# Kernel optimization log

Hardware: AMD Instinct MI355X
Metric: run time of the kernel (lower is better)

## Reference

```python
import jax, jax.numpy as jnp
import numpy as np

N, E, D, H, ED = 50000, 800000, 128, 4, 64
C = D // H  # per-head channels
EPS = 1e-5


def setup_inputs() -> dict:
    key = jax.random.key(0)
    ks = jax.random.split(key, 16)
    s = 0.05
    return {
        "x": jax.random.normal(ks[0], (N, D), jnp.float32),
        "edge_index": jax.random.randint(ks[1], (2, E), 0, N, jnp.int64 if jax.config.jax_enable_x64 else jnp.int32),
        "edge_attr": jax.random.normal(ks[2], (E, ED), jnp.float32),
        "Wq": jax.random.normal(ks[3], (D, H * C), jnp.float32) * s,
        "bq": jnp.zeros((H * C,), jnp.float32),
        "Wk": jax.random.normal(ks[4], (D, H * C), jnp.float32) * s,
        "bk": jnp.zeros((H * C,), jnp.float32),
        "Wv": jax.random.normal(ks[5], (D, H * C), jnp.float32) * s,
        "bv": jnp.zeros((H * C,), jnp.float32),
        "We": jax.random.normal(ks[6], (ED, H * C), jnp.float32) * s,  # lin_edge, bias=False
        "Wskip": jax.random.normal(ks[7], (D, H * C), jnp.float32) * s,
        "bskip": jnp.zeros((H * C,), jnp.float32),
        "Wbeta": jax.random.normal(ks[8], (3 * H * C, 1), jnp.float32) * s,  # lin_beta, bias=False
        "gamma": jnp.ones((D,), jnp.float32),
        "beta_ln": jnp.zeros((D,), jnp.float32),
    }


def _transformer_conv(x, src, dst, edge_attr, Wq, bq, Wk, bk, Wv, bv, We, Wskip, bskip, Wbeta):
    q = (x @ Wq + bq).reshape(N, H, C)
    k = (x @ Wk + bk).reshape(N, H, C)
    v = (x @ Wv + bv).reshape(N, H, C)
    e = (edge_attr @ We).reshape(E, H, C)
    k_j = k[src] + e                     # [E,H,C]
    v_j = v[src] + e                     # [E,H,C]
    alpha = jnp.einsum("ehc,ehc->eh", q[dst], k_j) / jnp.sqrt(jnp.float32(C))
    # per-destination softmax over incoming edges
    m = jax.ops.segment_max(alpha, dst, num_segments=N)          # [N,H]
    m = jnp.where(jnp.isfinite(m), m, 0.0)
    a = jnp.exp(alpha - m[dst])
    denom = jax.ops.segment_sum(a, dst, num_segments=N)          # [N,H]
    alpha = a / jnp.where(denom > 0, denom, 1.0)[dst]
    out = jax.ops.segment_sum(alpha[:, :, None] * v_j, dst, num_segments=N)  # [N,H,C]
    out = out.reshape(N, H * C)
    # beta-gated skip (beta=True, root_weight)
    x_r = x @ Wskip + bskip
    b = jax.nn.sigmoid(jnp.concatenate([out, x_r, out - x_r], axis=-1) @ Wbeta)  # [N,1]
    return b * x_r + (1.0 - b) * out


def reference(x, edge_index, edge_attr, Wq, bq, Wk, bk, Wv, bv, We, Wskip, bskip, Wbeta, gamma, beta_ln):
    src, dst = edge_index[0], edge_index[1]
    res = _transformer_conv(x, src, dst, edge_attr, Wq, bq, Wk, bk, Wv, bv, We, Wskip, bskip, Wbeta)
    out = jax.nn.gelu(res, approximate=False) + x
    mu = jnp.mean(out, axis=-1, keepdims=True)
    var = jnp.var(out, axis=-1, keepdims=True)
    return (out - mu) * jax.lax.rsqrt(var + EPS) * gamma + beta_ln
```

## Files before the change

### kernel.cpp

```cpp
#include <hip/hip_runtime.h>
#include <math.h>

#define NN 50000
#define EE 800000

typedef __bf16 bf16x8 __attribute__((ext_vector_type(8)));
typedef float f32x4 __attribute__((ext_vector_type(4)));
typedef float f32x2 __attribute__((ext_vector_type(2)));
typedef unsigned short ushort_t;
typedef unsigned int uint_t;

__device__ inline ushort_t f2bf(float f) {
  uint_t u = __float_as_uint(f);
  uint_t r = (u + 0x7fffu + ((u >> 16) & 1u)) >> 16;
  return (ushort_t)r;
}
__device__ inline float bflo(uint_t u) { return __uint_as_float(u << 16); }
__device__ inline float bfhi(uint_t u) { return __uint_as_float(u & 0xffff0000u); }

__device__ inline uint_t pk4_fp8(float a0, float a1, float a2, float a3) {
  a0 = fminf(fmaxf(a0, -448.f), 448.f);
  a1 = fminf(fmaxf(a1, -448.f), 448.f);
  a2 = fminf(fmaxf(a2, -448.f), 448.f);
  a3 = fminf(fmaxf(a3, -448.f), 448.f);
  uint_t lo = (uint_t)__builtin_amdgcn_cvt_pk_fp8_f32(a0, a1, 0, false) & 0xFFFFu;
  uint_t hi = (uint_t)__builtin_amdgcn_cvt_pk_fp8_f32(a2, a3, 0, false) & 0xFFFFu;
  return lo | (hi << 16);
}

__device__ inline void wave_sync() {
  asm volatile("s_waitcnt lgkmcnt(0)" ::: "memory");
  __builtin_amdgcn_wave_barrier();
}

__global__ __launch_bounds__(256) void k_prepA(const float* __restrict__ Wbeta,
                                               float* __restrict__ wcomb,
                                               int* __restrict__ counts) {
  int b = blockIdx.x;
  int o = threadIdx.x;
  if (b == 0) {
    if (o < 128) {
      wcomb[o]       = Wbeta[o]       + Wbeta[256 + o];
      wcomb[128 + o] = Wbeta[128 + o] - Wbeta[256 + o];
    }
  } else {
    int i = (b - 1) * 256 + o;
    if (i < NN) counts[i] = 0;
  }
}

__global__ __launch_bounds__(256) void k_prepB(
    const float* __restrict__ Wq, const float* __restrict__ Wk,
    const float* __restrict__ Wv, const float* __restrict__ Ws,
    const float* __restrict__ bq, const float* __restrict__ bk,
    const float* __restrict__ bv, const float* __restrict__ bs,
    ushort_t* __restrict__ Wbt, float* __restrict__ bcat,
    const float* __restrict__ We, ushort_t* __restrict__ WebT,
    const int* __restrict__ ei, int* __restrict__ counts) {
  int b = blockIdx.x;
  if (b >= 288) {
    int i = (b - 288) * 256 + threadIdx.x;
    if (i < EE) atomicAdd(&counts[ei[EE + i]], 1);
    return;
  }
  if (b >= 256) {
    int i = (b - 256) * 256 + threadIdx.x;
    int c = i >> 6, k = i & 63;
    WebT[c * 64 + k] = f2bf(We[k * 128 + c]);
    return;
  }
  int i = b * 256 + threadIdx.x;
  int c = i >> 7, k = i & 127;
  float w;
  if (c < 128)      w = Wq[k * 128 + c];
  else if (c < 256) w = Wk[k * 128 + (c - 128)];
  else if (c < 384) w = Wv[k * 128 + (c - 256)];
  else              w = Ws[k * 128 + (c - 384)];
  Wbt[(size_t)c * 128 + k] = f2bf(w);
  if (i < 512) {
    float bb;
    if (i < 128)      bb = bq[i];
    else if (i < 256) bb = bk[i - 128];
    else if (i < 384) bb = bv[i - 256];
    else              bb = bs[i - 384];
    bcat[i] = bb;
  }
}

__global__ __launch_bounds__(256) void k_mm(const float* __restrict__ x,
                                            const ushort_t* __restrict__ Wbt,
                                            const float* __restrict__ bcat,
                                            float* __restrict__ nqx,
                                            ushort_t* __restrict__ kb,
                                            ushort_t* __restrict__ vb) {
  __shared__ ushort_t As[128 * 128];
  __shared__ ushort_t Bs[128 * 128];
  int t = threadIdx.x;
  int rb = blockIdx.x * 128;
  int cb = blockIdx.y * 128;

  for (int q = t; q < 2048; q += 256) {
    int r = q >> 4, j = q & 15;
    int row = rb + r;
    float4 f0 = make_float4(0.f, 0.f, 0.f, 0.f), f1 = f0;
    if (row < NN) {
      const float4* xp = (const float4*)&x[(size_t)row * 128 + j * 8];
      f0 = xp[0]; f1 = xp[1];
    }
    uint_t u0 = (uint_t)f2bf(f0.x) | ((uint_t)f2bf(f0.y) << 16);
    uint_t u1 = (uint_t)f2bf(f0.z) | ((uint_t)f2bf(f0.w) << 16);
    uint_t u2 = (uint_t)f2bf(f1.x) | ((uint_t)f2bf(f1.y) << 16);
    uint_t u3 = (uint_t)f2bf(f1.z) | ((uint_t)f2bf(f1.w) << 16);
    int e = r * 128 + ((j * 8) ^ ((r & 7) << 3));
    *(uint4*)&As[e] = make_uint4(u0, u1, u2, u3);
  }
  for (int q = t; q < 2048; q += 256) {
    int c = q >> 4, j = q & 15;
    uint4 w = *(const uint4*)&Wbt[(size_t)(cb + c) * 128 + j * 8];
    int e = c * 128 + ((j * 8) ^ ((c & 7) << 3));
    *(uint4*)&Bs[e] = w;
  }
  __syncthreads();

  int lane = t & 63;
  int wv = t >> 6;
  int wr = wv >> 1, wc = wv & 1;
  int l15 = lane & 15, l4 = lane >> 4;

  f32x4 acc[4][4];
#pragma unroll
  for (int i = 0; i < 4; ++i)
#pragma unroll
    for (int j = 0; j < 4; ++j) acc[i][j] = (f32x4){0.f, 0.f, 0.f, 0.f};

#pragma unroll
  for (int ks = 0; ks < 4; ++ks) {
    int kbv = ks * 32 + l4 * 8;
    bf16x8 af[4], bfr[4];
#pragma unroll
    for (int i = 0; i < 4; ++i) {
      int r = wr * 64 + i * 16 + l15;
      af[i] = *(const bf16x8*)&As[r * 128 + (kbv ^ ((r & 7) << 3))];
    }
#pragma unroll
    for (int j = 0; j < 4; ++j) {
      int c = wc * 64 + j * 16 + l15;
      bfr[j] = *(const bf16x8*)&Bs[c * 128 + (kbv ^ ((c & 7) << 3))];
    }
#pragma unroll
    for (int i = 0; i < 4; ++i)
#pragma unroll
      for (int j = 0; j < 4; ++j)
        acc[i][j] = __builtin_amdgcn_mfma_f32_16x16x32_bf16(af[i], bfr[j], acc[i][j], 0, 0, 0);
  }

#pragma unroll
  for (int j = 0; j < 4; ++j) {
    int colg = cb + wc * 64 + j * 16 + l15;
    float bv = bcat[colg];
#pragma unroll
    for (int i = 0; i < 4; ++i) {
#pragma unroll
      for (int reg = 0; reg < 4; ++reg) {
        int grow = rb + wr * 64 + i * 16 + l4 * 4 + reg;
        if (grow < NN) {
          float val = acc[i][j][reg] + bv;
          if (cb == 0)        nqx[(size_t)grow * 256 + colg] = val;
          else if (cb == 128) kb[(size_t)grow * 128 + (colg - 128)] = f2bf(val);
          else if (cb == 256) vb[(size_t)grow * 128 + (colg - 256)] = f2bf(val);
          else                nqx[(size_t)grow * 256 + (colg - 256)] = val;
        }
      }
    }
  }
}

__global__ __launch_bounds__(1024) void k_scan(int* __restrict__ counts, int* __restrict__ offsets) {
  __shared__ int wsum[16];
  __shared__ int s_carry;
  int4* counts4 = (int4*)counts;
  int4* offsets4 = (int4*)offsets;
  int t = threadIdx.x, lane = t & 63, w = t >> 6;
  if (t == 0) s_carry = 0;
  __syncthreads();
  for (int base = 0; base < 12500; base += 1024) {
    int idx = base + t;
    int4 v = (idx < 12500) ? counts4[idx] : make_int4(0, 0, 0, 0);
    int e1 = v.x, e2 = e1 + v.y, e3 = e2 + v.z, tot = e3 + v.w;
    int s = tot;
#pragma unroll
    for (int off = 1; off < 64; off <<= 1) {
      int u = __shfl_up(s, off);
      if (lane >= off) s += u;
    }
    if (lane == 63) wsum[w] = s;
    __syncthreads();
    if (t == 0) {
      int ex = s_carry;
#pragma unroll
      for (int i = 0; i < 16; ++i) { int tv = wsum[i]; wsum[i] = ex; ex += tv; }
      s_carry = ex;
    }
    __syncthreads();
    int be = wsum[w] + s - tot;
    if (idx < 12500) {
      int4 o = make_int4(be, be + e1, be + e2, be + e3);
      offsets4[idx] = o;
      counts4[idx] = o;
    }
    __syncthreads();
  }
  if (t == 0) offsets[NN] = s_carry;
}

__global__ __launch_bounds__(256) void k_fillw(const int* __restrict__ ei,
                                               int* __restrict__ cursors,
                                               const float* __restrict__ ea,
                                               const ushort_t* __restrict__ WebT,
                                               int* __restrict__ srcs,
                                               unsigned char* __restrict__ eaWperm) {
  __shared__ ushort_t As[64 * 64];
  __shared__ ushort_t Bs[128 * 64];
  __shared__ int sP[64];
  int t = threadIdx.x;
  int eb = blockIdx.x * 64;

  if (t < 64) {
    int e = eb + t;
    int d = ei[EE + e];
    int p = atomicAdd(&cursors[d], 1);
    sP[t] = p;
    srcs[p] = ei[e];
  }
  for (int q = t; q < 512; q += 256) {
    int r = q >> 3, j = q & 7;
    const float4* xp = (const float4*)&ea[(size_t)(eb + r) * 64 + j * 8];
    float4 f0 = xp[0], f1 = xp[1];
    uint_t u0 = (uint_t)f2bf(f0.x) | ((uint_t)f2bf(f0.y) << 16);
    uint_t u1 = (uint_t)f2bf(f0.z) | ((uint_t)f2bf(f0.w) << 16);
    uint_t u2 = (uint_t)f2bf(f1.x) | ((uint_t)f2bf(f1.y) << 16);
    uint_t u3 = (uint_t)f2bf(f1.z) | ((uint_t)f2bf(f1.w) << 16);
    *(uint4*)&As[r * 64 + ((j * 8) ^ ((r & 7) << 3))] = make_uint4(u0, u1, u2, u3);
  }
  for (int q = t; q < 1024; q += 256) {
    int c = q >> 3, j = q & 7;
    uint4 w = *(const uint4*)&WebT[(size_t)c * 64 + j * 8];
    *(uint4*)&Bs[c * 64 + ((j * 8) ^ ((c & 7) << 3))] = w;
  }
  __syncthreads();

  int lane = t & 63, wv = t >> 6;
  int l15 = lane & 15, l4 = lane >> 4;
  int edge = wv * 16 + l15;

  bf16x8 bfr[2];
#pragma unroll
  for (int ks = 0; ks < 2; ++ks) {
    int kbv = ks * 32 + l4 * 8;
    bfr[ks] = *(const bf16x8*)&As[edge * 64 + (kbv ^ ((edge & 7) << 3))];
  }

  f32x4 acc[8];
#pragma unroll
  for (int i = 0; i < 8; ++i) acc[i] = (f32x4){0.f, 0.f, 0.f, 0.f};

#pragma unroll
  for (int ks = 0; ks < 2; ++ks) {
    int kbv = ks * 32 + l4 * 8;
#pragma unroll
    for (int i = 0; i < 8; ++i) {
      int c = i * 16 + l15;
      bf16x8 af = *(const bf16x8*)&Bs[c * 64 + (kbv ^ ((c & 7) << 3))];
      acc[i] = __builtin_amdgcn_mfma_f32_16x16x32_bf16(af, bfr[ks], acc[i], 0, 0, 0);
    }
  }

  wave_sync();
  uint_t* dst32 = (uint_t*)As;
#pragma unroll
  for (int i = 0; i < 8; ++i)
    dst32[edge * 32 + i * 4 + l4] = pk4_fp8(acc[i][0], acc[i][1], acc[i][2], acc[i][3]);
  wave_sync();

  int el = wv * 16 + (lane >> 2), seg = lane & 3;
  const uint4* srow = (const uint4*)((const unsigned char*)As + el * 128 + seg * 16);
  uint4 lo = srow[0];
  uint4 hi = srow[4];
  int p = sP[el];
  *(uint4*)&eaWperm[(size_t)p * 128 + seg * 16]      = lo;
  *(uint4*)&eaWperm[(size_t)p * 128 + seg * 16 + 64] = hi;
}

__global__ __launch_bounds__(256) void k_attn(
    const float* __restrict__ nqx,
    const ushort_t* __restrict__ kb, const ushort_t* __restrict__ vb,
    const unsigned char* __restrict__ eaWperm,
    const int* __restrict__ offsets, const int* __restrict__ srcs,
    const float* __restrict__ x, const float* __restrict__ wcomb,
    const float* __restrict__ gamma, const float* __restrict__ beta_ln,
    float* __restrict__ out) {
  __shared__ float sQ[4][128];
  __shared__ unsigned char sEA[4][16][144];
  __shared__ float sA[4][64];
  __shared__ int   sS[4][16];

  int t = threadIdx.x, wv = t >> 6, l = t & 63;
  int n = blockIdx.x * 4 + wv;
  int h = l >> 4, m = l & 15;
  int c0 = 2 * l, c1 = c0 + 1;
  const float scale = 0.17677669529663687f;

  const float* nrow = nqx + (size_t)n * 256;
  float2 q2 = *(const float2*)&nrow[c0];
  *(float2*)&sQ[wv][c0] = make_float2(q2.x * scale, q2.y * scale);
  if (l < 16) sS[wv][l] = 0;

  int js = offsets[n], je = offsets[n + 1];
  float acc0 = 0.f, acc1 = 0.f, lsum = 0.f;

  for (int base = js; base < je; base += 16) {
    int nj = je - base; if (nj > 16) nj = 16;
    wave_sync();

    uint4 e0 = {0,0,0,0}, e1 = {0,0,0,0};
    uint4 k0 = {0,0,0,0}, k1 = {0,0,0,0}, k2 = {0,0,0,0}, k3 = {0,0,0,0};
    if (m < nj) {
      int s = srcs[base + m];
      const uint4* erow = (const uint4*)(eaWperm + (size_t)(base + m) * 128 + 32 * h);
      e0 = erow[0]; e1 = erow[1];
      const uint4* krow = (const uint4*)(kb + (size_t)s * 128 + 32 * h);
      k0 = krow[0]; k1 = krow[1]; k2 = krow[2]; k3 = krow[3];
      if (h == 0) sS[wv][m] = s;
    }
    *(uint4*)&sEA[wv][m][32 * h]      = e0;
    *(uint4*)&sEA[wv][m][32 * h + 16] = e1;
    wave_sync();

    float z = 0.f;
    {
      const float* qp = &sQ[wv][32 * h];
      uint_t eu[8] = {e0.x, e0.y, e0.z, e0.w, e1.x, e1.y, e1.z, e1.w};
      uint_t ku[16] = {k0.x, k0.y, k0.z, k0.w, k1.x, k1.y, k1.z, k1.w,
                       k2.x, k2.y, k2.z, k2.w, k3.x, k3.y, k3.z, k3.w};
#pragma unroll
      for (int u = 0; u < 8; ++u) {
        f32x2 elo = __builtin_amdgcn_cvt_pk_f32_fp8(eu[u] & 0xFFFFu, false);
        f32x2 ehi = __builtin_amdgcn_cvt_pk_f32_fp8(eu[u] >> 16, false);
        float4 q4 = *(const float4*)&qp[4 * u];
        z += q4.x * (bflo(ku[2 * u]) + elo.x)
           + q4.y * (bfhi(ku[2 * u]) + elo.y)
           + q4.z * (bflo(ku[2 * u + 1]) + ehi.x)
           + q4.w * (bfhi(ku[2 * u + 1]) + ehi.y);
      }
    }
    float a = (m < nj) ? __expf(z) : 0.0f;
    lsum += a;
    sA[wv][l] = a;
    wave_sync();

    {
      int4 s0 = *(const int4*)&sS[wv][0];
      int4 s1 = *(const int4*)&sS[wv][4];
      f32x4 a0 = *(const f32x4*)&sA[wv][16 * h];
      f32x4 a1 = *(const f32x4*)&sA[wv][16 * h + 4];
      uint_t vv[8];
      int sidx[8] = {s0.x, s0.y, s0.z, s0.w, s1.x, s1.y, s1.z, s1.w};
#pragma unroll
      for (int e = 0; e < 8; ++e)
        vv[e] = *(const uint_t*)(vb + (size_t)sidx[e] * 128 + c0);
#pragma unroll
      for (int e = 0; e < 8; ++e) {
        float ae = (e < 4) ? a0[e] : a1[e - 4];
        uint_t ew = (uint_t)*(const ushort_t*)&sEA[wv][e][2 * l];
        f32x2 ef = __builtin_amdgcn_cvt_pk_f32_fp8(ew, false);
        acc0 += ae * (bflo(vv[e]) + ef.x);
        acc1 += ae * (bfhi(vv[e]) + ef.y);
      }
    }
    if (nj > 8) {
      int4 s2 = *(const int4*)&sS[wv][8];
      int4 s3 = *(const int4*)&sS[wv][12];
      f32x4 a2 = *(const f32x4*)&sA[wv][16 * h + 8];
      f32x4 a3 = *(const f32x4*)&sA[wv][16 * h + 12];
      uint_t vv[8];
      int sidx[8] = {s2.x, s2.y, s2.z, s2.w, s3.x, s3.y, s3.z, s3.w};
#pragma unroll
      for (int e = 0; e < 8; ++e)
        vv[e] = *(const uint_t*)(vb + (size_t)sidx[e] * 128 + c0);
#pragma unroll
      for (int e = 0; e < 8; ++e) {
        float ae = (e < 4) ? a2[e] : a3[e - 4];
        uint_t ew = (uint_t)*(const ushort_t*)&sEA[wv][8 + e][2 * l];
        f32x2 ef = __builtin_amdgcn_cvt_pk_f32_fp8(ew, false);
        acc0 += ae * (bflo(vv[e]) + ef.x);
        acc1 += ae * (bfhi(vv[e]) + ef.y);
      }
    }
  }

  lsum += __shfl_xor(lsum, 1); lsum += __shfl_xor(lsum, 2);
  lsum += __shfl_xor(lsum, 4); lsum += __shfl_xor(lsum, 8);

  float inv = (lsum > 0.f) ? (1.0f / lsum) : 1.0f;
  float o0 = acc0 * inv;
  float o1 = acc1 * inv;

  float2 xrv = *(const float2*)&nrow[128 + c0];
  float bp = o0 * wcomb[c0] + o1 * wcomb[c1] + xrv.x * wcomb[128 + c0] + xrv.y * wcomb[128 + c1];
#pragma unroll
  for (int off = 32; off > 0; off >>= 1) bp += __shfl_xor(bp, off);
  float bgate = 1.0f / (1.0f + __expf(-bp));
  float r0 = bgate * xrv.x + (1.0f - bgate) * o0;
  float r1 = bgate * xrv.y + (1.0f - bgate) * o1;

  float2 xv = *(const float2*)&x[(size_t)n * 128 + c0];
  float ge0 = 0.5f * r0 * (1.0f + erff(r0 * 0.70710678118654752f)) + xv.x;
  float ge1 = 0.5f * r1 * (1.0f + erff(r1 * 0.70710678118654752f)) + xv.y;

  float s1 = ge0 + ge1;
  float s2 = ge0 * ge0 + ge1 * ge1;
#pragma unroll
  for (int off = 32; off > 0; off >>= 1) {
    s1 += __shfl_xor(s1, off);
    s2 += __shfl_xor(s2, off);
  }
  float mean = s1 * (1.0f / 128.0f);
  float var = s2 * (1.0f / 128.0f) - mean * mean;
  float rstd = rsqrtf(var + 1e-5f);
  float2 ov;
  ov.x = (ge0 - mean) * rstd * gamma[c0] + beta_ln[c0];
  ov.y = (ge1 - mean) * rstd * gamma[c1] + beta_ln[c1];
  *(float2*)&out[(size_t)n * 128 + c0] = ov;
}

extern "C" void kernel_launch(void* const* d_in, const int* in_sizes, int n_in,
                              void* d_out, int out_size, void* d_ws, size_t ws_size,
                              hipStream_t stream) {
  const float* x   = (const float*)d_in[0];
  const int*   ei  = (const int*)d_in[1];
  const float* ea  = (const float*)d_in[2];
  const float* Wq  = (const float*)d_in[3];
  const float* bq  = (const float*)d_in[4];
  const float* Wk  = (const float*)d_in[5];
  const float* bk  = (const float*)d_in[6];
  const float* Wv  = (const float*)d_in[7];
  const float* bv  = (const float*)d_in[8];
  const float* We  = (const float*)d_in[9];
  const float* Wsk = (const float*)d_in[10];
  const float* bsk = (const float*)d_in[11];
  const float* Wb  = (const float*)d_in[12];
  const float* gamma = (const float*)d_in[13];
  const float* beta  = (const float*)d_in[14];
  float* out = (float*)d_out;

  char* cur = (char*)d_ws;
  auto alloc = [&](size_t bytes) {
    void* p = (void*)cur;
    cur += (bytes + 255) & ~(size_t)255;
    return p;
  };
  float*         nqx     = (float*)alloc((size_t)NN * 256 * 4);
  ushort_t*      kbuf    = (ushort_t*)alloc((size_t)NN * 128 * 2);
  ushort_t*      vbuf    = (ushort_t*)alloc((size_t)NN * 128 * 2);
  unsigned char* eaWperm = (unsigned char*)alloc((size_t)EE * 128);
  int*           srcs    = (int*)alloc((size_t)EE * 4);
  float*         wcomb   = (float*)alloc(256 * 4);
  float*         bcat    = (float*)alloc(512 * 4);
  ushort_t*      Wbt     = (ushort_t*)alloc((size_t)512 * 128 * 2);
  ushort_t*      WebT    = (ushort_t*)alloc((size_t)128 * 64 * 2);
  int*           counts  = (int*)alloc((size_t)NN * 4);
  int*           offsets = (int*)alloc((size_t)(NN + 4) * 4);

  k_prepA<<<197, 256, 0, stream>>>(Wb, wcomb, counts);
  k_prepB<<<288 + 3125, 256, 0, stream>>>(Wq, Wk, Wv, Wsk, bq, bk, bv, bsk,
                                          Wbt, bcat, We, WebT, ei, counts);
  k_mm<<<dim3(391, 4), 256, 0, stream>>>(x, Wbt, bcat, nqx, kbuf, vbuf);
  k_scan<<<1, 1024, 0, stream>>>(counts, offsets);
  k_fillw<<<12500, 256, 0, stream>>>(ei, counts, ea, WebT, srcs, eaWperm);
  k_attn<<<12500, 256, 0, stream>>>(nqx, kbuf, vbuf, eaWperm, offsets, srcs,
                                    x, wcomb, gamma, beta, out);
}
```

Baseline: 311.1 us.

## Store edge projections in original edge order and gather them via index pairs

k_fillw now writes the fp8 edge-attribute projections contiguously in original edge order and records a (edge id, src) pair at each CSR slot, replacing the scattered per-slot writes. The LDS staging buffer gets an XOR swizzle so the packed rows can be read back as coalesced 128-byte rows. k_attn then gathers each edge row through the stored edge id, trading coalesced writes in k_fillw for random 128-byte reads in k_attn and an 8-byte pair read per edge instead of 4 bytes.

```diff
diff --git a/kernel.cpp b/kernel.cpp
--- a/kernel.cpp
+++ b/kernel.cpp
@@ -217,11 +217,10 @@
                                                int* __restrict__ cursors,
                                                const float* __restrict__ ea,
                                                const ushort_t* __restrict__ WebT,
-                                               int* __restrict__ srcs,
-                                               unsigned char* __restrict__ eaWperm) {
+                                               int2* __restrict__ pairs,
+                                               unsigned char* __restrict__ eaW) {
   __shared__ ushort_t As[64 * 64];
   __shared__ ushort_t Bs[128 * 64];
-  __shared__ int sP[64];
   int t = threadIdx.x;
   int eb = blockIdx.x * 64;
 
@@ -229,8 +228,7 @@
     int e = eb + t;
     int d = ei[EE + e];
     int p = atomicAdd(&cursors[d], 1);
-    sP[t] = p;
-    srcs[p] = ei[e];
+    pairs[p] = make_int2(e, ei[e]);
   }
   for (int q = t; q < 512; q += 256) {
     int r = q >> 3, j = q & 7;
@@ -279,23 +277,29 @@
   uint_t* dst32 = (uint_t*)As;
 #pragma unroll
   for (int i = 0; i < 8; ++i)
-    dst32[edge * 32 + i * 4 + l4] = pk4_fp8(acc[i][0], acc[i][1], acc[i][2], acc[i][3]);
+    dst32[edge * 32 + ((i * 4 + l4) ^ ((edge & 7) << 2))] =
+        pk4_fp8(acc[i][0], acc[i][1], acc[i][2], acc[i][3]);
   wave_sync();
 
-  int el = wv * 16 + (lane >> 2), seg = lane & 3;
-  const uint4* srow = (const uint4*)((const unsigned char*)As + el * 128 + seg * 16);
-  uint4 lo = srow[0];
-  uint4 hi = srow[4];
-  int p = sP[el];
-  *(uint4*)&eaWperm[(size_t)p * 128 + seg * 16]      = lo;
-  *(uint4*)&eaWperm[(size_t)p * 128 + seg * 16 + 64] = hi;
+  {
+    int row = t >> 2;
+    int sw = (row & 7) << 2;
+    const uint_t* src32 = (const uint_t*)As + row * 32;
+    int w0 = ((t & 3) * 8) ^ sw;
+    int w1 = ((t & 3) * 8 + 4) ^ sw;
+    uint4 lo = *(const uint4*)&src32[w0];
+    uint4 hi = *(const uint4*)&src32[w1];
+    unsigned char* dst = eaW + (size_t)(eb + row) * 128 + (t & 3) * 32;
+    *(uint4*)dst = lo;
+    *(uint4*)(dst + 16) = hi;
+  }
 }
 
 __global__ __launch_bounds__(256) void k_attn(
     const float* __restrict__ nqx,
     const ushort_t* __restrict__ kb, const ushort_t* __restrict__ vb,
-    const unsigned char* __restrict__ eaWperm,
-    const int* __restrict__ offsets, const int* __restrict__ srcs,
+    const unsigned char* __restrict__ eaW,
+    const int* __restrict__ offsets, const int2* __restrict__ pairs,
     const float* __restrict__ x, const float* __restrict__ wcomb,
     const float* __restrict__ gamma, const float* __restrict__ beta_ln,
     float* __restrict__ out) {
@@ -325,12 +329,12 @@
     uint4 e0 = {0,0,0,0}, e1 = {0,0,0,0};
     uint4 k0 = {0,0,0,0}, k1 = {0,0,0,0}, k2 = {0,0,0,0}, k3 = {0,0,0,0};
     if (m < nj) {
-      int s = srcs[base + m];
-      const uint4* erow = (const uint4*)(eaWperm + (size_t)(base + m) * 128 + 32 * h);
+      int2 pr = pairs[base + m];
+      const uint4* erow = (const uint4*)(eaW + (size_t)pr.x * 128 + 32 * h);
       e0 = erow[0]; e1 = erow[1];
-      const uint4* krow = (const uint4*)(kb + (size_t)s * 128 + 32 * h);
+      const uint4* krow = (const uint4*)(kb + (size_t)pr.y * 128 + 32 * h);
       k0 = krow[0]; k1 = krow[1]; k2 = krow[2]; k3 = krow[3];
-      if (h == 0) sS[wv][m] = s;
+      if (h == 0) sS[wv][m] = pr.y;
     }
     *(uint4*)&sEA[wv][m][32 * h]      = e0;
     *(uint4*)&sEA[wv][m][32 * h + 16] = e1;
@@ -462,8 +466,8 @@
   float*         nqx     = (float*)alloc((size_t)NN * 256 * 4);
   ushort_t*      kbuf    = (ushort_t*)alloc((size_t)NN * 128 * 2);
   ushort_t*      vbuf    = (ushort_t*)alloc((size_t)NN * 128 * 2);
-  unsigned char* eaWperm = (unsigned char*)alloc((size_t)EE * 128);
-  int*           srcs    = (int*)alloc((size_t)EE * 4);
+  unsigned char* eaW     = (unsigned char*)alloc((size_t)EE * 128);
+  int2*          pairs   = (int2*)alloc((size_t)EE * 8);
   float*         wcomb   = (float*)alloc(256 * 4);
   float*         bcat    = (float*)alloc(512 * 4);
   ushort_t*      Wbt     = (ushort_t*)alloc((size_t)512 * 128 * 2);
@@ -476,7 +480,7 @@
                                           Wbt, bcat, We, WebT, ei, counts);
   k_mm<<<dim3(391, 4), 256, 0, stream>>>(x, Wbt, bcat, nqx, kbuf, vbuf);
   k_scan<<<1, 1024, 0, stream>>>(counts, offsets);
-  k_fillw<<<12500, 256, 0, stream>>>(ei, counts, ea, WebT, srcs, eaWperm);
-  k_attn<<<12500, 256, 0, stream>>>(nqx, kbuf, vbuf, eaWperm, offsets, srcs,
+  k_fillw<<<12500, 256, 0, stream>>>(ei, counts, ea, WebT, pairs, eaW);
+  k_attn<<<12500, 256, 0, stream>>>(nqx, kbuf, vbuf, eaW, offsets, pairs,
                                     x, wcomb, gamma, beta, out);
 }
```

Measured after the change: 321.2 us. 3.3% more time.

## Restructure edge-weight kernel: per-wave 64 edges, register-resident We fragments, no block sync

Applied to the files above, without the earlier changes.

Each wave now handles 64 edges in four groups of 16, so blocks cover 256 edges and the grid shrinks fourfold. The We fragments are loaded from global memory straight into registers once per wave and reused across the four groups. Edge features are converted to bf16 directly in registers instead of being staged through shared memory. This removes the block-wide barrier and the shared-memory staging of the A and B tiles, and amortises the weight loads over more edges. The costs are higher register pressure (16 weight fragments plus 8 edge fragments) and fewer blocks in the grid. The fp8 output is still transposed through a swizzled per-wave shared buffer, and each lane now writes two contiguous 16-byte chunks.

```diff
diff --git a/kernel.cpp b/kernel.cpp
--- a/kernel.cpp
+++ b/kernel.cpp
@@ -32,6 +32,8 @@
   asm volatile("s_waitcnt lgkmcnt(0)" ::: "memory");
   __builtin_amdgcn_wave_barrier();
 }
+
+union UB8 { uint4 u; bf16x8 v; };
 
 __global__ __launch_bounds__(256) void k_prepA(const float* __restrict__ Wbeta,
                                                float* __restrict__ wcomb,
@@ -219,76 +221,77 @@
                                                const ushort_t* __restrict__ WebT,
                                                int* __restrict__ srcs,
                                                unsigned char* __restrict__ eaWperm) {
-  __shared__ ushort_t As[64 * 64];
-  __shared__ ushort_t Bs[128 * 64];
-  __shared__ int sP[64];
-  int t = threadIdx.x;
-  int eb = blockIdx.x * 64;
-
-  if (t < 64) {
-    int e = eb + t;
+  __shared__ uint_t sOut[4][16 * 32];
+  __shared__ int sP[4][64];
+  int t = threadIdx.x, w = t >> 6, l = t & 63;
+  int l15 = l & 15, l4 = l >> 4;
+  int eb = blockIdx.x * 256 + w * 64;
+
+  {
+    int e = eb + l;
     int d = ei[EE + e];
     int p = atomicAdd(&cursors[d], 1);
-    sP[t] = p;
+    sP[w][l] = p;
     srcs[p] = ei[e];
   }
-  for (int q = t; q < 512; q += 256) {
-    int r = q >> 3, j = q & 7;
-    const float4* xp = (const float4*)&ea[(size_t)(eb + r) * 64 + j * 8];
-    float4 f0 = xp[0], f1 = xp[1];
-    uint_t u0 = (uint_t)f2bf(f0.x) | ((uint_t)f2bf(f0.y) << 16);
-    uint_t u1 = (uint_t)f2bf(f0.z) | ((uint_t)f2bf(f0.w) << 16);
-    uint_t u2 = (uint_t)f2bf(f1.x) | ((uint_t)f2bf(f1.y) << 16);
-    uint_t u3 = (uint_t)f2bf(f1.z) | ((uint_t)f2bf(f1.w) << 16);
-    *(uint4*)&As[r * 64 + ((j * 8) ^ ((r & 7) << 3))] = make_uint4(u0, u1, u2, u3);
-  }
-  for (int q = t; q < 1024; q += 256) {
-    int c = q >> 3, j = q & 7;
-    uint4 w = *(const uint4*)&WebT[(size_t)c * 64 + j * 8];
-    *(uint4*)&Bs[c * 64 + ((j * 8) ^ ((c & 7) << 3))] = w;
-  }
-  __syncthreads();
-
-  int lane = t & 63, wv = t >> 6;
-  int l15 = lane & 15, l4 = lane >> 4;
-  int edge = wv * 16 + l15;
-
-  bf16x8 bfr[2];
-#pragma unroll
-  for (int ks = 0; ks < 2; ++ks) {
-    int kbv = ks * 32 + l4 * 8;
-    bfr[ks] = *(const bf16x8*)&As[edge * 64 + (kbv ^ ((edge & 7) << 3))];
-  }
-
-  f32x4 acc[8];
-#pragma unroll
-  for (int i = 0; i < 8; ++i) acc[i] = (f32x4){0.f, 0.f, 0.f, 0.f};
-
-#pragma unroll
-  for (int ks = 0; ks < 2; ++ks) {
-    int kbv = ks * 32 + l4 * 8;
+
+  bf16x8 bf[4][2];
+#pragma unroll
+  for (int g = 0; g < 4; ++g) {
+    const float* er = ea + (size_t)(eb + g * 16 + l15) * 64;
+#pragma unroll
+    for (int ks = 0; ks < 2; ++ks) {
+      const float4* p4 = (const float4*)(er + ks * 32 + l4 * 8);
+      float4 f0 = p4[0], f1 = p4[1];
+      UB8 ub;
+      ub.u.x = (uint_t)f2bf(f0.x) | ((uint_t)f2bf(f0.y) << 16);
+      ub.u.y = (uint_t)f2bf(f0.z) | ((uint_t)f2bf(f0.w) << 16);
+      ub.u.z = (uint_t)f2bf(f1.x) | ((uint_t)f2bf(f1.y) << 16);
+      ub.u.w = (uint_t)f2bf(f1.z) | ((uint_t)f2bf(f1.w) << 16);
+      bf[g][ks] = ub.v;
+    }
+  }
+
+  bf16x8 wf[2][8];
+#pragma unroll
+  for (int ks = 0; ks < 2; ++ks)
 #pragma unroll
     for (int i = 0; i < 8; ++i) {
       int c = i * 16 + l15;
-      bf16x8 af = *(const bf16x8*)&Bs[c * 64 + (kbv ^ ((c & 7) << 3))];
-      acc[i] = __builtin_amdgcn_mfma_f32_16x16x32_bf16(af, bfr[ks], acc[i], 0, 0, 0);
-    }
-  }
-
-  wave_sync();
-  uint_t* dst32 = (uint_t*)As;
-#pragma unroll
-  for (int i = 0; i < 8; ++i)
-    dst32[edge * 32 + i * 4 + l4] = pk4_fp8(acc[i][0], acc[i][1], acc[i][2], acc[i][3]);
-  wave_sync();
-
-  int el = wv * 16 + (lane >> 2), seg = lane & 3;
-  const uint4* srow = (const uint4*)((const unsigned char*)As + el * 128 + seg * 16);
-  uint4 lo = srow[0];
-  uint4 hi = srow[4];
-  int p = sP[el];
-  *(uint4*)&eaWperm[(size_t)p * 128 + seg * 16]      = lo;
-  *(uint4*)&eaWperm[(size_t)p * 128 + seg * 16 + 64] = hi;
+      wf[ks][i] = *(const bf16x8*)&WebT[c * 64 + ks * 32 + l4 * 8];
+    }
+
+#pragma unroll
+  for (int g = 0; g < 4; ++g) {
+    f32x4 acc[8];
+#pragma unroll
+    for (int i = 0; i < 8; ++i) acc[i] = (f32x4){0.f, 0.f, 0.f, 0.f};
+#pragma unroll
+    for (int ks = 0; ks < 2; ++ks)
+#pragma unroll
+      for (int i = 0; i < 8; ++i)
+        acc[i] = __builtin_amdgcn_mfma_f32_16x16x32_bf16(wf[ks][i], bf[g][ks], acc[i], 0, 0, 0);
+
+    wave_sync();
+    uint_t* dst = &sOut[w][0];
+#pragma unroll
+    for (int i = 0; i < 8; ++i)
+      dst[l15 * 32 + ((i * 4 + l4) ^ ((l15 & 7) << 2))] =
+          pk4_fp8(acc[i][0], acc[i][1], acc[i][2], acc[i][3]);
+    wave_sync();
+
+    int row = l >> 2;
+    int sw = (row & 7) << 2;
+    const uint_t* src32 = &sOut[w][row * 32];
+    int w0 = ((l & 3) * 8) ^ sw;
+    int w1 = ((l & 3) * 8 + 4) ^ sw;
+    uint4 lo = *(const uint4*)&src32[w0];
+    uint4 hi = *(const uint4*)&src32[w1];
+    int p = sP[w][g * 16 + row];
+    unsigned char* dstg = eaWperm + (size_t)p * 128 + (l & 3) * 32;
+    *(uint4*)dstg = lo;
+    *(uint4*)(dstg + 16) = hi;
+  }
 }
 
 __global__ __launch_bounds__(256) void k_attn(
@@ -476,7 +479,7 @@
                                           Wbt, bcat, We, WebT, ei, counts);
   k_mm<<<dim3(391, 4), 256, 0, stream>>>(x, Wbt, bcat, nqx, kbuf, vbuf);
   k_scan<<<1, 1024, 0, stream>>>(counts, offsets);
-  k_fillw<<<12500, 256, 0, stream>>>(ei, counts, ea, WebT, srcs, eaWperm);
+  k_fillw<<<3125, 256, 0, stream>>>(ei, counts, ea, WebT, srcs, eaWperm);
   k_attn<<<12500, 256, 0, stream>>>(nqx, kbuf, vbuf, eaWperm, offsets, srcs,
                                     x, wcomb, gamma, beta, out);
 }
```

After: 315.5 us. No clear change (+1.4%).
